# Kernel optimization log

Hardware: AMD Instinct MI355X
Metric: run time of the kernel (lower is better)

## Reference

```python
import jax, jax.numpy as jnp
import numpy as np

B, C, D, H, W, K = 2, 192, 48, 48, 48, 7
EPS_LN = 1e-6
EPS_GRN = 1e-6


def setup_inputs() -> dict:
    key = jax.random.key(0)
    ks = jax.random.split(key, 8)
    sc = 0.02
    return {
        "x": jax.random.normal(ks[0], (B, C, D, H, W), jnp.float32),
        # depthwise conv kernel in DHWIO layout: [K,K,K,1,C] (torch weight [C,1,K,K,K])
        "conv_w": jax.random.normal(ks[1], (K, K, K, 1, C), jnp.float32) * sc,
        "conv_b": jnp.zeros((C,), jnp.float32),
        "ln_g": jnp.ones((C,), jnp.float32),
        "ln_b": jnp.zeros((C,), jnp.float32),
        "w1": jax.random.normal(ks[2], (C, 4 * C), jnp.float32) * sc,
        "b1": jnp.zeros((4 * C,), jnp.float32),
        "grn_gamma": jax.random.normal(ks[3], (4 * C,), jnp.float32) * sc,
        "grn_beta": jax.random.normal(ks[4], (4 * C,), jnp.float32) * sc,
        "w2": jax.random.normal(ks[5], (4 * C, C), jnp.float32) * sc,
        "b2": jnp.zeros((C,), jnp.float32),
    }


def reference(x, conv_w, conv_b, ln_g, ln_b, w1, b1, grn_gamma, grn_beta, w2, b2):
    c = x.shape[1]
    # NCDHW -> NDHWC (channels-last, as Permute([0,2,3,4,1]) after the conv)
    xc = jnp.transpose(x, (0, 2, 3, 4, 1))
    # depthwise conv3d, kernel 7, pad 3 (SAME for stride 1)
    y = jax.lax.conv_general_dilated(
        xc, conv_w, window_strides=(1, 1, 1), padding="SAME",
        dimension_numbers=("NDHWC", "DHWIO", "NDHWC"),
        feature_group_count=c,
    ) + conv_b
    # LayerNorm over channel dim, eps=1e-6 (biased variance, like torch)
    mu = jnp.mean(y, axis=-1, keepdims=True)
    var = jnp.mean(jnp.square(y - mu), axis=-1, keepdims=True)
    y = (y - mu) * jax.lax.rsqrt(var + EPS_LN) * ln_g + ln_b
    # MLP up + exact GELU
    y = jax.nn.gelu(y @ w1 + b1, approximate=False)
    # GRN: global L2 over spatial dims per channel
    gx = jnp.sqrt(jnp.sum(y * y, axis=(1, 2, 3), keepdims=True))  # [B,1,1,1,4C]
    nx = gx / (jnp.mean(gx, axis=-1, keepdims=True) + EPS_GRN)
    y = grn_gamma * (y * nx) + grn_beta + y
    # MLP down, permute back, residual
    y = y @ w2 + b2
    return jnp.transpose(y, (0, 4, 1, 2, 3)) + x
```

## Files before the change

### kernel.cpp

```cpp
#include <hip/hip_runtime.h>
#include <math.h>

#define Bn 2
#define Cn 192
#define Dn 48
#define Hn 48
#define Wn 48
#define C4 768
#define DHW (Dn*Hn*Wn)
#define CDHW ((long)Cn*DHW)

typedef __attribute__((ext_vector_type(8))) short bf16x8;
typedef __attribute__((ext_vector_type(4))) float f32x4;

__device__ inline float bf2f(unsigned short u) {
    union { float f; unsigned int i; } v; v.i = ((unsigned int)u) << 16; return v.f;
}
__device__ inline unsigned short f2bf(float f) {
    union { float f; unsigned int i; } v; v.f = f;
    unsigned int r = v.i + 0x7FFFu + ((v.i >> 16) & 1u);
    return (unsigned short)(r >> 16);
}
__device__ inline float blo(unsigned int u) {
    union { unsigned int i; float f; } v; v.i = u << 16; return v.f;
}
__device__ inline float bhi(unsigned int u) {
    union { unsigned int i; float f; } v; v.i = u & 0xffff0000u; return v.f;
}
__device__ inline unsigned int cvtpk_bf16(float lo, float hi) {
    unsigned int r;
    asm("v_cvt_pk_bf16_f32 %0, %1, %2" : "=v"(r) : "v"(lo), "v"(hi));
    return r;
}
__device__ inline float gelu_tanh(float v) {
    float u = v * fmaf(0.0356774081f, v * v, 0.7978845608f);
    float a = fabsf(u);
    float t = __expf(-2.0f * a);
    float th = (1.0f - t) / (1.0f + t);
    th = copysignf(th, u);
    return 0.5f * v * (1.0f + th);
}

__global__ __launch_bounds__(256)
void xpad_k(const float* __restrict__ x, unsigned short* __restrict__ xbf)
{
    int u = blockIdx.x * 256 + threadIdx.x;
    int j = u & 7;
    int row = u >> 3;
    unsigned short* orow = xbf + ((size_t)row << 6);
    uint4 o = {0u, 0u, 0u, 0u};
    if (j >= 1 && j <= 6) {
        const float* xr = x + (size_t)row * 48 + (8 * j - 8);
        float4 a = *(const float4*)xr;
        float4 b = *(const float4*)(xr + 4);
        o.x = cvtpk_bf16(a.x, a.y); o.y = cvtpk_bf16(a.z, a.w);
        o.z = cvtpk_bf16(b.x, b.y); o.w = cvtpk_bf16(b.z, b.w);
    }
    *(uint4*)(orow + 8 * j) = o;
}

__global__ __launch_bounds__(256)
void btoep_k(const float* __restrict__ cw, unsigned short* __restrict__ btp)
{
    int idx = blockIdx.x * 256 + threadIdx.x;
    int lane = idx & 63;
    int t = idx >> 6;
    int kdkh = t % 49, c = t / 49;
    int n = lane & 15, g = lane >> 4;
    unsigned short v[8];
#pragma unroll
    for (int j = 0; j < 8; ++j) {
        int kw = 8 * g + j - n - 5;
        v[j] = (kw >= 0 && kw <= 6) ? f2bf(cw[(kdkh * 7 + kw) * Cn + c])
                                    : (unsigned short)0;
    }
    *(uint4*)(btp + (size_t)idx * 8) = *(uint4*)v;
}

#define CTD 16
#define CHD (CTD+6)
#define CHH 22

__global__ __launch_bounds__(128)
void conv_dw(const unsigned short* __restrict__ xbf, const unsigned short* __restrict__ btp,
             const float* __restrict__ cb, unsigned short* __restrict__ yc)
{
    __shared__ unsigned int xt[CHD * CHH * 16];
    int c = blockIdx.y;
    int s = blockIdx.x;
    int wt = s % 3, ht = (s / 3) % 3, dt = s / 9;
    int d0 = dt * 16, h0 = ht * 16, w0 = wt * 16;
    int tid = threadIdx.x;

    const unsigned short* xc = xbf + ((size_t)c * 2304 << 6);
    for (int u = tid; u < CHD * CHH * 4; u += 128) {
        int g = u & 3, r2 = u >> 2;
        int hh2 = r2 % CHH, dd = r2 / CHH;
        int gd = d0 - 3 + dd, gh = h0 - 3 + hh2;
        uint4 v = {0u, 0u, 0u, 0u};
        if ((unsigned)gd < 48u && (unsigned)gh < 48u)
            v = *(const uint4*)(xc + (((size_t)gd * 48 + gh) << 6) + w0 + 8 * g);
        *(uint4*)&xt[(r2 << 4) + ((g ^ (r2 & 3)) << 2)] = v;
    }
    __syncthreads();

    int lane = tid & 63, wv = tid >> 6;
    int lr = lane & 15, g = lane >> 4;
    float bias = cb[c];
    f32x4 acc[8];
#pragma unroll
    for (int t = 0; t < 8; ++t) acc[t] = (f32x4){bias, bias, bias, bias};

    const unsigned short* bchan = btp + (size_t)c * 49 * 512;
    const unsigned short* xt16 = (const unsigned short*)xt;

    for (int kh = 0; kh < 7; ++kh) {
        bf16x8 Bf[7];
#pragma unroll
        for (int kd = 0; kd < 7; ++kd)
            Bf[kd] = *(const bf16x8*)(bchan + (size_t)((kd * 7 + kh) * 64 + lane) * 8);
#pragma unroll
        for (int p = 0; p < 14; ++p) {
            int r2 = (8 * wv + p) * CHH + kh + lr;
            bf16x8 Af = *(const bf16x8*)(xt16 + (r2 << 5) + ((g ^ (r2 & 3)) << 3));
#pragma unroll
            for (int kd = 0; kd < 7; ++kd) {
                int t = p - kd;
                if (t < 0 || t > 7) continue;
                acc[t] = __builtin_amdgcn_mfma_f32_16x16x32_bf16(Af, Bf[kd], acc[t], 0, 0, 0);
            }
        }
    }

    unsigned short* yb = yc + (long)c * DHW;
#pragma unroll
    for (int t = 0; t < 8; ++t) {
        int d = d0 + 8 * wv + t;
#pragma unroll
        for (int i = 0; i < 4; ++i) {
            int h = h0 + g * 4 + i;
            yb[((long)d * 48 + h) * 48 + w0 + lr] = f2bf(acc[t][i]);
        }
    }
}

__global__ __launch_bounds__(256)
void ln_kernel(const unsigned short* __restrict__ yc, const float* __restrict__ g,
               const float* __restrict__ lb, unsigned short* __restrict__ y1)
{
    __shared__ float tile[Cn * Wn];
    __shared__ float qs1[4][48], qs2[4][48];
    __shared__ float mu_s[Wn], rs_s[Wn];
    int dh = blockIdx.x;
    long rowbase = (long)dh * Wn;
    for (int l = threadIdx.x; l < Cn * 24; l += 256) {
        int c = l / 24, wp = l % 24;
        unsigned int u = *(const unsigned int*)&yc[rowbase + (long)c * DHW + wp * 2];
        tile[c * Wn + wp * 2]     = blo(u);
        tile[c * Wn + wp * 2 + 1] = bhi(u);
    }
    __syncthreads();
    if (threadIdx.x < 192) {
        int w = threadIdx.x >> 2, q = threadIdx.x & 3;
        float s1 = 0.f, s2 = 0.f;
        for (int cc = 0; cc < 48; ++cc) {
            float v = tile[(cc * 4 + q) * Wn + w];
            s1 += v; s2 = fmaf(v, v, s2);
        }
        qs1[q][w] = s1; qs2[q][w] = s2;
    }
    __syncthreads();
    if (threadIdx.x < 48) {
        int w = threadIdx.x;
        float s1 = qs1[0][w] + qs1[1][w] + qs1[2][w] + qs1[3][w];
        float s2 = qs2[0][w] + qs2[1][w] + qs2[2][w] + qs2[3][w];
        float mu = s1 * (1.0f / Cn);
        float var = s2 * (1.0f / Cn) - mu * mu;
        mu_s[w] = mu;
        rs_s[w] = rsqrtf(var + 1e-6f);
    }
    __syncthreads();
    long obase = (long)dh * Wn * Cn;
    for (int l = threadIdx.x; l < Cn * Wn; l += 256) {
        int w = l / Cn, c = l % Cn;
        float val = (tile[c * Wn + w] - mu_s[w]) * rs_s[w] * g[c] + lb[c];
        y1[obase + l] = f2bf(val);
    }
}

__global__ __launch_bounds__(256)
void wtrans(const float* __restrict__ W, unsigned short* __restrict__ Wt, int K, int N)
{
    int idx = blockIdx.x * 256 + threadIdx.x;
    if (idx >= K * N) return;
    int n = idx / K, k = idx % K;
    Wt[idx] = f2bf(W[(long)k * N + n]);
}

__global__ __launch_bounds__(256)
void wscale(const float* __restrict__ W2, const float* __restrict__ gx2,
            const float* __restrict__ gamma, unsigned short* __restrict__ W2s)
{
    __shared__ float red[256];
    int t = threadIdx.x;
    float s = 0.f;
#pragma unroll
    for (int i = 0; i < 3; ++i) s += sqrtf(gx2[t + i * 256]);
    red[t] = s; __syncthreads();
    for (int st = 128; st > 0; st >>= 1) {
        if (t < st) red[t] += red[t + st];
        __syncthreads();
    }
    float inv = 1.0f / (red[0] * (1.0f / C4) + 1e-6f);
    int idx = blockIdx.x * 256 + t;
    int n = idx / C4, k = idx % C4;
    float snx = 1.0f + gamma[k] * sqrtf(gx2[k]) * inv;
    W2s[idx] = f2bf(W2[(long)k * Cn + n] * snx);
}

#define BM 128
#define BN 64
#define BK 64

#define GEMM_STAGE(Aptr, Astride, Btptr, Bstride)                               \
    {                                                                           \
        _Pragma("unroll")                                                       \
        for (int i = 0; i < 4; ++i) {                                           \
            int chunk = i * 256 + tid;                                          \
            int r = chunk >> 3, cc = chunk & 7;                                 \
            bf16x8 v = *(const bf16x8*)((Aptr) + (size_t)(m0 + r) * (Astride) + k0 + cc * 8); \
            *(bf16x8*)&Asm[r * BK + ((cc ^ (r & 7)) * 8)] = v;                  \
        }                                                                       \
        _Pragma("unroll")                                                       \
        for (int i = 0; i < 2; ++i) {                                           \
            int chunk = i * 256 + tid;                                          \
            int r = chunk >> 3, cc = chunk & 7;                                 \
            bf16x8 v = *(const bf16x8*)((Btptr) + (size_t)(n0 + r) * (Bstride) + k0 + cc * 8); \
            *(bf16x8*)&Bsm[r * BK + ((cc ^ (r & 7)) * 8)] = v;                  \
        }                                                                       \
    }

#define GEMM_COMPUTE                                                            \
    _Pragma("unroll")                                                           \
    for (int kk = 0; kk < 2; ++kk) {                                            \
        bf16x8 af[4], bfr[2];                                                   \
        _Pragma("unroll")                                                       \
        for (int mi = 0; mi < 4; ++mi) {                                        \
            int r = wm * 64 + mi * 16 + lr;                                     \
            int cc = (kk * 4 + lq) ^ (r & 7);                                   \
            af[mi] = *(const bf16x8*)&Asm[r * BK + cc * 8];                     \
        }                                                                       \
        _Pragma("unroll")                                                       \
        for (int ni = 0; ni < 2; ++ni) {                                        \
            int r = wn * 32 + ni * 16 + lr;                                     \
            int cc = (kk * 4 + lq) ^ (r & 7);                                   \
            bfr[ni] = *(const bf16x8*)&Bsm[r * BK + cc * 8];                    \
        }                                                                       \
        _Pragma("unroll")                                                       \
        for (int mi = 0; mi < 4; ++mi)                                          \
            _Pragma("unroll")                                                   \
            for (int ni = 0; ni < 2; ++ni)                                      \
                acc[mi][ni] = __builtin_amdgcn_mfma_f32_16x16x32_bf16(          \
                    af[mi], bfr[ni], acc[mi][ni], 0, 0, 0);                     \
    }

__global__ __launch_bounds__(256)
void gemm_up(const unsigned short* __restrict__ A, const unsigned short* __restrict__ Bt,
             const float* __restrict__ bias, unsigned short* __restrict__ Y2,
             float* __restrict__ partial)
{
    __shared__ short Asm[BM * BK];
    __shared__ short Bsm[BN * BK];
    __shared__ float colred[BN];
    int tid = threadIdx.x;
    int lane = tid & 63, wv = tid >> 6;
    int wm = wv >> 1, wn = wv & 1;
    int lr = lane & 15, lq = lane >> 4;
    long m0 = (long)blockIdx.y * BM;
    int n0 = blockIdx.x * BN;

    f32x4 acc[4][2];
#pragma unroll
    for (int mi = 0; mi < 4; ++mi)
#pragma unroll
        for (int ni = 0; ni < 2; ++ni) acc[mi][ni] = (f32x4){0.f, 0.f, 0.f, 0.f};

    for (int k0 = 0; k0 < Cn; k0 += BK) {
        GEMM_STAGE(A, Cn, Bt, Cn);
        __syncthreads();
        GEMM_COMPUTE;
        __syncthreads();
    }

    unsigned short* yt = (unsigned short*)Asm;
    float ss[2] = {0.f, 0.f};
#pragma unroll
    for (int mi = 0; mi < 4; ++mi) {
#pragma unroll
        for (int ni = 0; ni < 2; ++ni) {
            int col = wn * 32 + ni * 16 + lr;
            float bb = bias[n0 + col];
            int row0 = wm * 64 + mi * 16 + lq * 4;
#pragma unroll
            for (int i = 0; i < 4; ++i) {
                float v = gelu_tanh(acc[mi][ni][i] + bb);
                ss[ni] = fmaf(v, v, ss[ni]);
                int row = row0 + i;
                yt[row * 64 + (col ^ ((row & 7) << 3))] = f2bf(v);
            }
        }
    }
#pragma unroll
    for (int ni = 0; ni < 2; ++ni) {
        ss[ni] += __shfl_xor(ss[ni], 16);
        ss[ni] += __shfl_xor(ss[ni], 32);
    }
    if (wm == 0 && lq == 0) {
        colred[wn * 32 + lr]      = ss[0];
        colred[wn * 32 + 16 + lr] = ss[1];
    }
    __syncthreads();
    if (wm == 1 && lq == 0) {
        colred[wn * 32 + lr]      += ss[0];
        colred[wn * 32 + 16 + lr] += ss[1];
    }
#pragma unroll
    for (int q = 0; q < 4; ++q) {
        int row = q * 32 + (tid >> 3);
        int cch = tid & 7;
        uint4 v = *(const uint4*)&yt[row * 64 + (cch ^ (row & 7)) * 8];
        *(uint4*)&Y2[(m0 + row) * C4 + n0 + cch * 8] = v;
    }
    __syncthreads();
    if (tid < BN) partial[(size_t)blockIdx.y * C4 + n0 + tid] = colred[tid];
}

__global__ __launch_bounds__(256)
void gemm_down(const unsigned short* __restrict__ A, const unsigned short* __restrict__ Bt,
               const float* __restrict__ beff, const float* __restrict__ x,
               float* __restrict__ out)
{
    __shared__ short Asm[BM * BK];
    __shared__ short Bsm[BN * BK];
    int tid = threadIdx.x;
    int lane = tid & 63, wv = tid >> 6;
    int wm = wv >> 1, wn = wv & 1;
    int lr = lane & 15, lq = lane >> 4;
    long m0 = (long)blockIdx.y * BM;
    int n0 = blockIdx.x * BN;

    f32x4 acc[4][2];
#pragma unroll
    for (int mi = 0; mi < 4; ++mi)
#pragma unroll
        for (int ni = 0; ni < 2; ++ni) acc[mi][ni] = (f32x4){0.f, 0.f, 0.f, 0.f};

    for (int k0 = 0; k0 < C4; k0 += BK) {
        GEMM_STAGE(A, C4, Bt, C4);
        __syncthreads();
        GEMM_COMPUTE;
        __syncthreads();
    }

#pragma unroll
    for (int mi = 0; mi < 4; ++mi) {
#pragma unroll
        for (int ni = 0; ni < 2; ++ni) {
            int colg = n0 + wn * 32 + ni * 16 + lr;
            float be = beff[colg];
            long mbase = m0 + wm * 64 + mi * 16 + lq * 4;
            const float* xp = x + (long)colg * DHW + mbase;
            float* op = out + (long)colg * DHW + mbase;
            float4 xvv = *(const float4*)xp;
            float4 o;
            o.x = acc[mi][ni][0] + be + xvv.x;
            o.y = acc[mi][ni][1] + be + xvv.y;
            o.z = acc[mi][ni][2] + be + xvv.z;
            o.w = acc[mi][ni][3] + be + xvv.w;
            *(float4*)op = o;
        }
    }
}

__global__ __launch_bounds__(256)
void grn_reduce(const float* __restrict__ partial, float* __restrict__ gx2)
{
    int n = blockIdx.x;
    const float* p = partial + n;
    float s = 0.f;
    for (int r = threadIdx.x; r < 864; r += 256) s += p[(long)r * C4];
    __shared__ float red[256];
    red[threadIdx.x] = s; __syncthreads();
    for (int st = 128; st > 0; st >>= 1) {
        if (threadIdx.x < st) red[threadIdx.x] += red[threadIdx.x + st];
        __syncthreads();
    }
    if (threadIdx.x == 0) gx2[n] = red[0];
}

__global__ __launch_bounds__(256)
void bias_eff_k(const float* __restrict__ beta, const float* __restrict__ W2,
                const float* __restrict__ b2, float* __restrict__ beff)
{
    __shared__ float red[256];
    int j = blockIdx.x, t = threadIdx.x;
    float s = 0.f;
#pragma unroll
    for (int i = 0; i < 3; ++i) {
        int k = t + i * 256;
        s = fmaf(beta[k], W2[(long)k * Cn + j], s);
    }
    red[t] = s; __syncthreads();
    for (int st = 128; st > 0; st >>= 1) {
        if (t < st) red[t] += red[t + st];
        __syncthreads();
    }
    if (t == 0) beff[j] = red[0] + b2[j];
}

extern "C" void kernel_launch(void* const* d_in, const int* in_sizes, int n_in,
                              void* d_out, int out_size, void* d_ws, size_t ws_size,
                              hipStream_t stream) {
    const float* x      = (const float*)d_in[0];
    const float* conv_w = (const float*)d_in[1];
    const float* conv_b = (const float*)d_in[2];
    const float* ln_g   = (const float*)d_in[3];
    const float* ln_b   = (const float*)d_in[4];
    const float* w1     = (const float*)d_in[5];
    const float* b1     = (const float*)d_in[6];
    const float* gg     = (const float*)d_in[7];
    const float* gb     = (const float*)d_in[8];
    const float* w2     = (const float*)d_in[9];
    const float* b2     = (const float*)d_in[10];
    float* out = (float*)d_out;
    char* ws = (char*)d_ws;

    unsigned short* yc  = (unsigned short*)(ws);
    unsigned short* xbf = (unsigned short*)(ws + 42467328L);
    unsigned short* y2  = (unsigned short*)(ws);
    unsigned short* y1  = (unsigned short*)(ws + 169869312L);
    unsigned short* btp = (unsigned short*)(ws + 202702848L);
    float*     partial  = (float*)(ws + 212336640L);
    unsigned short* w1t = (unsigned short*)(ws + 214990848L);
    unsigned short* w2s = (unsigned short*)(ws + 215285760L);
    float*         gx2  = (float*)(ws + 215580672L);
    float*        beff  = (float*)(ws + 215586816L);

    bias_eff_k<<<Cn, 256, 0, stream>>>(gb, w2, b2, beff);
    wtrans<<<(Cn * C4 + 255) / 256, 256, 0, stream>>>(w1, w1t, Cn, C4);

    for (int b = 0; b < Bn; ++b) {
        const float* xb = x + (size_t)b * CDHW;
        float* outb = out + (size_t)b * CDHW;
        xpad_k<<<(Cn * 2304 * 8) / 256, 256, 0, stream>>>(xb, xbf);
        btoep_k<<<(Cn * 49 * 64) / 256, 256, 0, stream>>>(conv_w, btp);
        dim3 gc(27, Cn);
        conv_dw<<<gc, 128, 0, stream>>>(xbf, btp, conv_b, yc);
        ln_kernel<<<Dn * Hn, 256, 0, stream>>>(yc, ln_g, ln_b, y1);
        dim3 gu(C4 / BN, DHW / BM);
        gemm_up<<<gu, 256, 0, stream>>>(y1, w1t, b1, y2, partial);
        grn_reduce<<<C4, 256, 0, stream>>>(partial, gx2);
        wscale<<<(Cn * C4) / 256, 256, 0, stream>>>(w2, gx2, gg, w2s);
        dim3 gd(Cn / BN, DHW / BM);
        gemm_down<<<gd, 256, 0, stream>>>(y2, w2s, beff, xb, outb);
    }
}
```

Baseline: 832.7 us.

## Keep full A row-tile resident in LDS and sweep all N tiles in gemm_up

gemm_up is restructured so each block loads one 128x192 A tile into LDS once and loops over all twelve 64-column N tiles. B fragments are read straight from global memory (expected to hit in L2) instead of being staged in LDS. The aim is to stop re-reading A for every N tile and to drop the per-k-step syncthreads. In exchange, Y2 is now written with scattered 2-byte stores instead of coalesced 16-byte stores, the LDS footprint per block is larger, and the grid is 12x smaller, which may lower occupancy and expose B load latency.

```diff
diff --git a/kernel.cpp b/kernel.cpp
--- a/kernel.cpp
+++ b/kernel.cpp
@@ -216,6 +216,89 @@
     int n = idx / C4, k = idx % C4;
     float snx = 1.0f + gamma[k] * sqrtf(gx2[k]) * inv;
     W2s[idx] = f2bf(W2[(long)k * Cn + n] * snx);
+}
+
+__global__ __launch_bounds__(256)
+void gemm_up(const unsigned short* __restrict__ A, const unsigned short* __restrict__ Bt,
+             const float* __restrict__ bias, unsigned short* __restrict__ Y2,
+             float* __restrict__ partial)
+{
+    __shared__ short Asm[128 * Cn];
+    __shared__ float colsum[2][C4];
+    int tid = threadIdx.x;
+    int lane = tid & 63, wv = tid >> 6;
+    int wm = wv >> 1, wn = wv & 1;
+    int lr = lane & 15, lq = lane >> 4;
+    long m0 = (long)blockIdx.x * 128;
+
+#pragma unroll
+    for (int i = 0; i < 12; ++i) {
+        int chunk = i * 256 + tid;
+        int r = chunk / 24, cc = chunk - r * 24;
+        bf16x8 v = *(const bf16x8*)(A + (size_t)(m0 + r) * Cn + cc * 8);
+        *(bf16x8*)&Asm[r * Cn + ((cc ^ (r & 7)) * 8)] = v;
+    }
+    __syncthreads();
+
+    for (int nt = 0; nt < 12; ++nt) {
+        int n0 = nt * 64;
+        f32x4 acc[4][2];
+#pragma unroll
+        for (int mi = 0; mi < 4; ++mi)
+#pragma unroll
+            for (int ni = 0; ni < 2; ++ni) acc[mi][ni] = (f32x4){0.f, 0.f, 0.f, 0.f};
+
+#pragma unroll
+        for (int ks = 0; ks < 6; ++ks) {
+            bf16x8 af[4], bfr[2];
+#pragma unroll
+            for (int ni = 0; ni < 2; ++ni) {
+                int nrow = n0 + wn * 32 + ni * 16 + lr;
+                bfr[ni] = *(const bf16x8*)(Bt + (size_t)nrow * Cn + (ks * 4 + lq) * 8);
+            }
+#pragma unroll
+            for (int mi = 0; mi < 4; ++mi) {
+                int r = wm * 64 + mi * 16 + lr;
+                int cc = (ks * 4 + lq) ^ (r & 7);
+                af[mi] = *(const bf16x8*)&Asm[r * Cn + cc * 8];
+            }
+#pragma unroll
+            for (int mi = 0; mi < 4; ++mi)
+#pragma unroll
+                for (int ni = 0; ni < 2; ++ni)
+                    acc[mi][ni] = __builtin_amdgcn_mfma_f32_16x16x32_bf16(
+                        af[mi], bfr[ni], acc[mi][ni], 0, 0, 0);
+        }
+
+        float ss[2] = {0.f, 0.f};
+#pragma unroll
+        for (int mi = 0; mi < 4; ++mi) {
+#pragma unroll
+            for (int ni = 0; ni < 2; ++ni) {
+                int col = wn * 32 + ni * 16 + lr;
+                float bb = bias[n0 + col];
+                long row0 = m0 + wm * 64 + mi * 16 + lq * 4;
+#pragma unroll
+                for (int i = 0; i < 4; ++i) {
+                    float v = gelu_tanh(acc[mi][ni][i] + bb);
+                    ss[ni] = fmaf(v, v, ss[ni]);
+                    Y2[(row0 + i) * C4 + n0 + col] = f2bf(v);
+                }
+            }
+        }
+#pragma unroll
+        for (int ni = 0; ni < 2; ++ni) {
+            ss[ni] += __shfl_xor(ss[ni], 16);
+            ss[ni] += __shfl_xor(ss[ni], 32);
+        }
+        if (lq == 0) {
+            colsum[wm][n0 + wn * 32 + lr]      = ss[0];
+            colsum[wm][n0 + wn * 32 + 16 + lr] = ss[1];
+        }
+    }
+    __syncthreads();
+    for (int i = tid; i < C4; i += 256)
+        partial[(size_t)blockIdx.x * C4 + i] = colsum[0][i] + colsum[1][i];
 }
 
 #define BM 128
@@ -265,77 +348,6 @@
     }
 
 __global__ __launch_bounds__(256)
-void gemm_up(const unsigned short* __restrict__ A, const unsigned short* __restrict__ Bt,
-             const float* __restrict__ bias, unsigned short* __restrict__ Y2,
-             float* __restrict__ partial)
-{
-    __shared__ short Asm[BM * BK];
-    __shared__ short Bsm[BN * BK];
-    __shared__ float colred[BN];
-    int tid = threadIdx.x;
-    int lane = tid & 63, wv = tid >> 6;
-    int wm = wv >> 1, wn = wv & 1;
-    int lr = lane & 15, lq = lane >> 4;
-    long m0 = (long)blockIdx.y * BM;
-    int n0 = blockIdx.x * BN;
-
-    f32x4 acc[4][2];
-#pragma unroll
-    for (int mi = 0; mi < 4; ++mi)
-#pragma unroll
-        for (int ni = 0; ni < 2; ++ni) acc[mi][ni] = (f32x4){0.f, 0.f, 0.f, 0.f};
-
-    for (int k0 = 0; k0 < Cn; k0 += BK) {
-        GEMM_STAGE(A, Cn, Bt, Cn);
-        __syncthreads();
-        GEMM_COMPUTE;
-        __syncthreads();
-    }
-
-    unsigned short* yt = (unsigned short*)Asm;
-    float ss[2] = {0.f, 0.f};
-#pragma unroll
-    for (int mi = 0; mi < 4; ++mi) {
-#pragma unroll
-        for (int ni = 0; ni < 2; ++ni) {
-            int col = wn * 32 + ni * 16 + lr;
-            float bb = bias[n0 + col];
-            int row0 = wm * 64 + mi * 16 + lq * 4;
-#pragma unroll
-            for (int i = 0; i < 4; ++i) {
-                float v = gelu_tanh(acc[mi][ni][i] + bb);
-                ss[ni] = fmaf(v, v, ss[ni]);
-                int row = row0 + i;
-                yt[row * 64 + (col ^ ((row & 7) << 3))] = f2bf(v);
-            }
-        }
-    }
-#pragma unroll
-    for (int ni = 0; ni < 2; ++ni) {
-        ss[ni] += __shfl_xor(ss[ni], 16);
-        ss[ni] += __shfl_xor(ss[ni], 32);
-    }
-    if (wm == 0 && lq == 0) {
-        colred[wn * 32 + lr]      = ss[0];
-        colred[wn * 32 + 16 + lr] = ss[1];
-    }
-    __syncthreads();
-    if (wm == 1 && lq == 0) {
-        colred[wn * 32 + lr]      += ss[0];
-        colred[wn * 32 + 16 + lr] += ss[1];
-    }
-#pragma unroll
-    for (int q = 0; q < 4; ++q) {
-        int row = q * 32 + (tid >> 3);
-        int cch = tid & 7;
-        uint4 v = *(const uint4*)&yt[row * 64 + (cch ^ (row & 7)) * 8];
-        *(uint4*)&Y2[(m0 + row) * C4 + n0 + cch * 8] = v;
-    }
-    __syncthreads();
-    if (tid < BN) partial[(size_t)blockIdx.y * C4 + n0 + tid] = colred[tid];
-}
-
-__global__ __launch_bounds__(256)
 void gemm_down(const unsigned short* __restrict__ A, const unsigned short* __restrict__ Bt,
                const float* __restrict__ beff, const float* __restrict__ x,
                float* __restrict__ out)
@@ -457,8 +469,7 @@
         dim3 gc(27, Cn);
         conv_dw<<<gc, 128, 0, stream>>>(xbf, btp, conv_b, yc);
         ln_kernel<<<Dn * Hn, 256, 0, stream>>>(yc, ln_g, ln_b, y1);
-        dim3 gu(C4 / BN, DHW / BM);
-        gemm_up<<<gu, 256, 0, stream>>>(y1, w1t, b1, y2, partial);
+        gemm_up<<<DHW / 128, 256, 0, stream>>>(y1, w1t, b1, y2, partial);
         grn_reduce<<<C4, 256, 0, stream>>>(partial, gx2);
         wscale<<<(Cn * C4) / 256, 256, 0, stream>>>(w2, gx2, gg, w2s);
         dim3 gd(Cn / BN, DHW / BM);
```

After: 806.5 us. 1.03x faster.
